# Kernel tuning notes

Measured on AMD Instinct MI355X. Metric: run time of the kernel, lower is better.

Reference implementation:

```python
import jax, jax.numpy as jnp
import numpy as np

B, T, V, E, H, S, C, VF, A, L = 32, 32, 32000, 512, 512, 512, 256, 512, 256, 50


def setup_inputs() -> dict:
    key = jax.random.key(0)
    ks = jax.random.split(key, 17)
    sc = lambda k, shp, fan: (jax.random.normal(k, shp, jnp.float32) / np.sqrt(fan)).astype(jnp.float32)
    inp = {
        "tgt": jax.random.randint(ks[0], (B, T), 0, V, dtype=jnp.int64),
        "decoder_state": jax.random.normal(ks[1], (B, H), jnp.float32),
        "category": jax.random.normal(ks[2], (B, C), jnp.float32),
        "v_feature": jax.random.normal(ks[3], (B, VF), jnp.float32),
        "session_outputs": jax.random.normal(ks[4], (B, L, S), jnp.float32),
        "session_mask": jnp.ones((B, L), dtype=bool),
        # learned parameters
        "emb": sc(ks[5], (V, E), E),
        "attn_Wh": sc(ks[6], (H, A), H),
        "attn_Ws": sc(ks[7], (S, A), S),
        "attn_b": jnp.zeros((A,), jnp.float32),
        "attn_v": sc(ks[8], (A,), A),
        "W_ih": sc(ks[9], (3 * H, E + S + C + VF), H),
        "W_hh": sc(ks[10], (3 * H, H), H),
        "b_ih": jnp.zeros((3 * H,), jnp.float32),
        "b_hh": jnp.zeros((3 * H,), jnp.float32),
        "W_out": 0.1 * jax.random.normal(ks[11], (V, H), jnp.float32),  # init.normal_(0, 0.1)
        "b_out": jnp.zeros((V,), jnp.float32),
    }
    return inp


def reference(tgt, decoder_state, category, v_feature, session_outputs, session_mask,
              emb, attn_Wh, attn_Ws, attn_b, attn_v, W_ih, W_hh, b_ih, b_hh, W_out, b_out):
    neg = jnp.finfo(session_outputs.dtype).min
    x = jnp.swapaxes(emb[tgt], 0, 1)                       # T,B,E
    sess_proj = jnp.einsum('bls,sa->bla', session_outputs, attn_Ws) + attn_b  # precompute key proj

    def step(h, x_t):
        # additive (Bahdanau) session attention on last-layer state h: B,H
        q = (h @ attn_Wh)[:, None, :]                      # B,1,A
        e = jnp.einsum('bla,a->bl', jnp.tanh(q + sess_proj), attn_v)
        e = jnp.where(session_mask, e, neg)
        a = jax.nn.softmax(e, axis=-1)                     # B,L
        ctx = jnp.einsum('bl,blh->bh', a, session_outputs)
        inp = jnp.concatenate([x_t, ctx, category, v_feature], axis=-1)
        # single-step GRU (PyTorch gate order: reset, update, new)
        gx = inp @ W_ih.T + b_ih
        gh = h @ W_hh.T + b_hh
        xr, xz, xn = jnp.split(gx, 3, axis=-1)
        hr, hz, hn = jnp.split(gh, 3, axis=-1)
        r = jax.nn.sigmoid(xr + hr)
        z = jax.nn.sigmoid(xz + hz)
        n = jnp.tanh(xn + r * hn)
        h2 = (1.0 - z) * n + z * h
        vocab = h2 @ W_out.T + b_out
        return h2, (vocab, h2)

    _, (vocab_outputs, outputs) = jax.lax.scan(step, decoder_state, x)
    return jnp.swapaxes(vocab_outputs, 0, 1), jnp.swapaxes(outputs, 0, 1)
```

## Files before the change

### kernel.cpp

```cpp
#include <hip/hip_runtime.h>

typedef unsigned short u16;
typedef unsigned int u32;
typedef __attribute__((ext_vector_type(8))) short short8;
typedef __attribute__((ext_vector_type(4))) float f32x4;

#define NB 32
#define NT 32
#define NV 32000
#define NE 512
#define NH 512
#define NS 512
#define NC 256
#define NVF 512
#define NA 256
#define NL 50
#define G3 1536
#define KG 1024
#define NG 2048

__device__ __forceinline__ float bf2f(u16 u) {
  union { u32 i; float f; } v; v.i = ((u32)u) << 16; return v.f;
}
__device__ __forceinline__ u16 f2bf(float f) {
  union { float f; u32 i; } v; v.f = f;
  u32 x = v.i;
  return (u16)((x + 0x7fffu + ((x >> 16) & 1u)) >> 16);
}
__device__ __forceinline__ float sigmoidf_(float x) { return 1.f / (1.f + __expf(-x)); }
__device__ __forceinline__ float tanhf_(float x) {
  x = fminf(fmaxf(x, -15.f), 15.f);
  float e = __expf(2.f * x);
  return (e - 1.f) / (e + 1.f);
}
__device__ __forceinline__ void cvt8(u16* dst, const float* src) {
  f32x4 a = *(const f32x4*)src;
  f32x4 b = *(const f32x4*)(src + 4);
  short8 o;
  o[0] = (short)f2bf(a[0]); o[1] = (short)f2bf(a[1]);
  o[2] = (short)f2bf(a[2]); o[3] = (short)f2bf(a[3]);
  o[4] = (short)f2bf(b[0]); o[5] = (short)f2bf(b[1]);
  o[6] = (short)f2bf(b[2]); o[7] = (short)f2bf(b[3]);
  *(short8*)dst = o;
}

__global__ __launch_bounds__(256) void prep_kernel(
    const int* __restrict__ tgt, const float* __restrict__ dec,
    const float* __restrict__ cat, const float* __restrict__ vfe,
    const float* __restrict__ sess, const float* __restrict__ emb,
    const float* __restrict__ Ws, const float* __restrict__ Wih,
    const float* __restrict__ Whh, const float* __restrict__ Wout,
    u16* __restrict__ Wg, u16* __restrict__ Wx, u16* __restrict__ X,
    float* __restrict__ h_ws, u16* __restrict__ Wob, u16* __restrict__ Wst,
    u16* __restrict__ sessb, u16* __restrict__ Wcv, u16* __restrict__ cvb)
{
  int blk = blockIdx.x, tid = threadIdx.x;
  if (blk < 1024) {
    int base = (blk * 256 + tid) * 8, j = base >> 10, c = base & 1023;
    if (j < G3 && c < 512)            cvt8(Wg + base, Whh + (size_t)j * 512 + c);
    else if (j < 1024 && c >= 512)    cvt8(Wg + base, Wih + (size_t)j * 1792 + c);
    else if (j >= G3 && c >= 512)     cvt8(Wg + base, Wih + (size_t)(j - 512) * 1792 + c);
    else                              *(short8*)(Wg + base) = (short8){0,0,0,0,0,0,0,0};
  } else if (blk < 1408) {
    int base = ((blk - 1024) * 256 + tid) * 8, j = base >> 9, c = base & 511;
    cvt8(Wx + base, Wih + (size_t)j * 1792 + c);
  } else if (blk < 1664) {
    int base = ((blk - 1408) * 256 + tid) * 8, tb = base >> 9, e = base & 511;
    cvt8(X + base, emb + (size_t)tgt[tb] * NE + e);
  } else if (blk < 1672) {
    int base = ((blk - 1664) * 256 + tid) * 8;
    *(f32x4*)(h_ws + base) = *(const f32x4*)(dec + base);
    *(f32x4*)(h_ws + base + 4) = *(const f32x4*)(dec + base + 4);
  } else if (blk < 9672) {
    int base = ((blk - 1672) * 256 + tid) * 8;
    cvt8(Wob + base, Wout + base);
  } else if (blk < 9736) {
    int base = ((blk - 9672) * 256 + tid) * 8, a = base >> 9, s = base & 511;
    short8 o;
    #pragma unroll
    for (int j = 0; j < 8; j++) o[j] = (short)f2bf(Ws[(size_t)(s + j) * NA + a]);
    *(short8*)(Wst + base) = o;
  } else if (blk < 10136) {
    int base = ((blk - 9736) * 256 + tid) * 8;
    cvt8(sessb + base, sess + base);
  } else if (blk < 10712) {
    int base = ((blk - 10136) * 256 + tid) * 8, j = base / 768, c = base % 768;
    cvt8(Wcv + base, Wih + (size_t)j * 1792 + 1024 + c);
  } else {
    int base = ((blk - 10712) * 256 + tid) * 8, b = base / 768, c = base % 768;
    if (c < NC) cvt8(cvb + base, cat + (size_t)b * NC + c);
    else        cvt8(cvb + base, vfe + (size_t)b * NVF + (c - NC));
  }
}

__global__ __launch_bounds__(256) void att_step(
    int t,
    const float* __restrict__ sess, const float* __restrict__ Wh,
    const float* __restrict__ av, const float* __restrict__ bhh,
    const float* __restrict__ sp, const float* __restrict__ gstat,
    const float* __restrict__ gx, const float* __restrict__ g,
    float* __restrict__ h_ws, u16* __restrict__ A_cur,
    float* __restrict__ h_out, u16* __restrict__ h_bf)
{
  int b = blockIdx.x, tid = threadIdx.x;
  __shared__ float h_s[512];
  __shared__ float qp[2048];
  __shared__ float q_s[256];
  __shared__ float e_s[64];
  __shared__ float a_s[64];

  if (t == 0) {
    h_s[tid] = h_ws[b * NH + tid];
    h_s[256 + tid] = h_ws[b * NH + 256 + tid];
  } else {
    const float* gxr = gx + ((size_t)b * NT + (t - 1)) * G3;
    const float* gr = g + (size_t)b * NG;
    const float* gsr = gstat + (size_t)b * G3;
    #pragma unroll
    for (int s = 0; s < 2; s++) {
      int k = tid + s * 256;
      float hprev = h_ws[b * NH + k];
      float rr = sigmoidf_(gxr[k] + gsr[k] + gr[k] + bhh[k]);
      float zz = sigmoidf_(gxr[512 + k] + gsr[512 + k] + gr[512 + k] + bhh[512 + k]);
      float hn = gr[1024 + k] + bhh[1024 + k];
      float xn = gxr[1024 + k] + gsr[1024 + k] + gr[1536 + k];
      float nn = tanhf_(xn + rr * hn);
      float h2 = (1.f - zz) * nn + zz * hprev;
      h_s[k] = h2;
      h_ws[b * NH + k] = h2;
      h_out[((size_t)b * NT + (t - 1)) * NH + k] = h2;
      h_bf[((size_t)b * NT + (t - 1)) * NH + k] = f2bf(h2);
    }
  }
  __syncthreads();
  if (t == NT) return;

  A_cur[b * KG + tid] = f2bf(h_s[tid]);
  A_cur[b * KG + 256 + tid] = f2bf(h_s[256 + tid]);

  {
    int grp = tid >> 5, lb = tid & 31;
    float qa[8] = {0.f,0.f,0.f,0.f,0.f,0.f,0.f,0.f};
    for (int hh = grp * 64; hh < grp * 64 + 64; hh++) {
      float hv = h_s[hh];
      const float* wr = Wh + (size_t)hh * NA + lb * 8;
      f32x4 w0 = *(const f32x4*)wr;
      f32x4 w1 = *(const f32x4*)(wr + 4);
      qa[0] += hv * w0[0]; qa[1] += hv * w0[1]; qa[2] += hv * w0[2]; qa[3] += hv * w0[3];
      qa[4] += hv * w1[0]; qa[5] += hv * w1[1]; qa[6] += hv * w1[2]; qa[7] += hv * w1[3];
    }
    #pragma unroll
    for (int j = 0; j < 8; j++) qp[grp * 256 + lb * 8 + j] = qa[j];
  }
  __syncthreads();
  {
    float qq = 0.f;
    #pragma unroll
    for (int gg = 0; gg < 8; gg++) qq += qp[gg * 256 + tid];
    q_s[tid] = qq;
  }
  __syncthreads();

  if (tid < 200) {
    int l2 = tid >> 2, grp = tid & 3;
    const float* spr = sp + ((size_t)b * NL + l2) * NA + grp * 64;
    const float* avp = av + grp * 64;
    float part = 0.f;
    for (int j = 0; j < 64; j++)
      part += tanhf_(q_s[grp * 64 + j] + spr[j]) * avp[j];
    part += __shfl_xor(part, 1);
    part += __shfl_xor(part, 2);
    if (grp == 0) e_s[l2] = part;
  }
  __syncthreads();
  if (tid < 64) {
    float x = (tid < NL) ? e_s[tid] : -3.0e38f;
    float m = x;
    #pragma unroll
    for (int o = 1; o < 64; o <<= 1) m = fmaxf(m, __shfl_xor(m, o));
    float p = (tid < NL) ? __expf(x - m) : 0.f;
    float ssum = p;
    #pragma unroll
    for (int o = 1; o < 64; o <<= 1) ssum += __shfl_xor(ssum, o);
    a_s[tid] = p / ssum;
  }
  __syncthreads();

  #pragma unroll
  for (int s0 = 0; s0 < 2; s0++) {
    int s = tid + s0 * 256;
    float acc = 0.f;
    for (int l = 0; l < NL; l++)
      acc += a_s[l] * sess[((size_t)b * NL + l) * NS + s];
    A_cur[b * KG + 512 + s] = f2bf(acc);
  }
}

template<int BM, bool BIAS>
__global__ __launch_bounds__(256) void gemm_bt(
    const u16* __restrict__ Aw, int lda, const u16* __restrict__ Bw, int ldb,
    float* __restrict__ Cw, int ldc, const float* __restrict__ bias, int K, int nblk)
{
  int bn = blockIdx.x % nblk, bm = blockIdx.x / nblk;
  int w = threadIdx.x >> 6, l = threadIdx.x & 63;
  int lr = l & 15, kb = (l >> 4) * 8, r0 = (l >> 4) * 4;
  int n0 = bn * 64 + w * 16;
  constexpr int MT = BM / 16;
  f32x4 acc[MT];
  #pragma unroll
  for (int i = 0; i < MT; i++) acc[i] = (f32x4){0.f, 0.f, 0.f, 0.f};
  const u16* bp = Bw + (size_t)(n0 + lr) * ldb + kb;
  const u16* ap = Aw + (size_t)(bm * BM + lr) * lda + kb;
  #pragma unroll 4
  for (int k0 = 0; k0 < K; k0 += 32) {
    short8 bfr = *(const short8*)(bp + k0);
    #pragma unroll
    for (int mt = 0; mt < MT; mt++) {
      short8 afr = *(const short8*)(ap + (size_t)mt * 16 * lda + k0);
      acc[mt] = __builtin_amdgcn_mfma_f32_16x16x32_bf16(afr, bfr, acc[mt], 0, 0, 0);
    }
  }
  int col = n0 + lr;
  float bv = 0.f;
  if constexpr (BIAS) bv = bias[col];
  #pragma unroll
  for (int mt = 0; mt < MT; mt++) {
    #pragma unroll
    for (int i = 0; i < 4; i++) {
      int row = bm * BM + mt * 16 + r0 + i;
      Cw[(size_t)row * ldc + col] = acc[mt][i] + bv;
    }
  }
}

__global__ __launch_bounds__(256) void vocab_gemm(
    const u16* __restrict__ Aw, const u16* __restrict__ Bw,
    const float* __restrict__ bias, float* __restrict__ Cw)
{
  int bm = blockIdx.x / 250, bn = blockIdx.x % 250;
  int w = threadIdx.x >> 6, l = threadIdx.x & 63;
  int lr = l & 15, kb = (l >> 4) * 8, r0 = (l >> 4) * 4;
  __shared__ __align__(16) u16 As[128 * 136];
  f32x4 acc[8][2];
  #pragma unroll
  for (int i = 0; i < 8; i++) { acc[i][0] = (f32x4){0.f,0.f,0.f,0.f}; acc[i][1] = (f32x4){0.f,0.f,0.f,0.f}; }
  int n0 = bn * 128;
  const u16* bp0 = Bw + (size_t)(n0 + w * 16 + lr) * 512 + kb;
  const u16* bp1 = Bw + (size_t)(n0 + 64 + w * 16 + lr) * 512 + kb;
  for (int ko = 0; ko < 512; ko += 128) {
    __syncthreads();
    #pragma unroll
    for (int it = 0; it < 8; it++) {
      int idx = it * 256 + (int)threadIdx.x;
      int row = idx >> 4, c8 = (idx & 15) * 8;
      *(short8*)(As + row * 136 + c8) = *(const short8*)(Aw + (size_t)(bm * 128 + row) * 512 + ko + c8);
    }
    __syncthreads();
    #pragma unroll
    for (int kc = 0; kc < 128; kc += 32) {
      short8 bf0 = *(const short8*)(bp0 + ko + kc);
      short8 bf1 = *(const short8*)(bp1 + ko + kc);
      #pragma unroll
      for (int mt = 0; mt < 8; mt++) {
        short8 afr = *(const short8*)(As + (mt * 16 + lr) * 136 + kc + kb);
        acc[mt][0] = __builtin_amdgcn_mfma_f32_16x16x32_bf16(afr, bf0, acc[mt][0], 0, 0, 0);
        acc[mt][1] = __builtin_amdgcn_mfma_f32_16x16x32_bf16(afr, bf1, acc[mt][1], 0, 0, 0);
      }
    }
  }
  int col0 = n0 + w * 16 + lr, col1 = col0 + 64;
  float bv0 = bias[col0], bv1 = bias[col1];
  #pragma unroll
  for (int mt = 0; mt < 8; mt++) {
    #pragma unroll
    for (int i = 0; i < 4; i++) {
      int row = bm * 128 + mt * 16 + r0 + i;
      Cw[(size_t)row * NV + col0] = acc[mt][0][i] + bv0;
      Cw[(size_t)row * NV + col1] = acc[mt][1][i] + bv1;
    }
  }
}

extern "C" void kernel_launch(void* const* d_in, const int* in_sizes, int n_in,
                              void* d_out, int out_size, void* d_ws, size_t ws_size,
                              hipStream_t stream)
{
  const int* tgt = (const int*)d_in[0];
  const float* dec = (const float*)d_in[1];
  const float* cat = (const float*)d_in[2];
  const float* vfe = (const float*)d_in[3];
  const float* sess = (const float*)d_in[4];
  const float* emb = (const float*)d_in[6];
  const float* Wh = (const float*)d_in[7];
  const float* Ws = (const float*)d_in[8];
  const float* ab = (const float*)d_in[9];
  const float* av = (const float*)d_in[10];
  const float* Wih = (const float*)d_in[11];
  const float* Whh = (const float*)d_in[12];
  const float* bih = (const float*)d_in[13];
  const float* bhh = (const float*)d_in[14];
  const float* Wout = (const float*)d_in[15];
  const float* bout = (const float*)d_in[16];

  float* out_vocab = (float*)d_out;
  float* h_out = out_vocab + (size_t)NB * NT * NV;

  float* sp = (float*)d_ws;
  float* gstat = sp + NB * NL * NA;
  float* gx = gstat + NB * G3;
  float* g = gx + (size_t)NB * NT * G3;
  float* h_ws = g + NB * NG;
  u16* Wg = (u16*)(h_ws + NB * NH);
  u16* Wx = Wg + (size_t)NG * KG;
  u16* X = Wx + (size_t)G3 * NE;
  u16* A_cur = X + (size_t)NB * NT * NE;
  u16* h_bf = A_cur + NB * KG;
  u16* Wob = h_bf + (size_t)NB * NT * NH;
  u16* Wst = Wob + (size_t)NV * NH;
  u16* sessb = Wst + (size_t)NA * NS;
  u16* Wcv = sessb + (size_t)NB * NL * NS;
  u16* cvb = Wcv + (size_t)G3 * 768;

  prep_kernel<<<10724, 256, 0, stream>>>(tgt, dec, cat, vfe, sess, emb, Ws, Wih, Whh, Wout,
                                         Wg, Wx, X, h_ws, Wob, Wst, sessb, Wcv, cvb);
  gemm_bt<64, false><<<16 * 24, 256, 0, stream>>>(X, 512, Wx, 512, gx, G3, nullptr, 512, 24);
  gemm_bt<64, true><<<25 * 4, 256, 0, stream>>>(sessb, 512, Wst, 512, sp, NA, ab, 512, 4);
  gemm_bt<32, true><<<24, 256, 0, stream>>>(cvb, 768, Wcv, 768, gstat, G3, bih, 768, 24);
  for (int t = 0; t < NT; t++) {
    att_step<<<NB, 256, 0, stream>>>(t, sess, Wh, av, bhh, sp, gstat, gx, g, h_ws, A_cur, h_out, h_bf);
    gemm_bt<32, false><<<32, 256, 0, stream>>>(A_cur, KG, Wg, KG, g, NG, nullptr, KG, 32);
  }
  att_step<<<NB, 256, 0, stream>>>(NT, sess, Wh, av, bhh, sp, gstat, gx, g, h_ws, A_cur, h_out, h_bf);
  vocab_gemm<<<8 * 250, 256, 0, stream>>>(h_bf, Wob, bout, out_vocab);
}
```

Before: 1.348 ms.

## Precompute session-context gate projection and merge query projection into recurrent GEMM

Uses the linearity of the context term to precompute session_outputs @ W_ih[:,512:1024]^T per session position as a bf16 tensor. Each step then mixes these projected rows with the attention weights instead of forming the context and multiplying it by W_ih. The attention query projection W_h is appended to the recurrent GEMM weight, so one GEMM with K=512 yields both the hidden gates and q, shrinking the per-step GEMM from K=1024/N=2048. The vocab GEMM is also retiled to direct-from-global fragments with an LDS-staged coalesced epilogue. The risks are extra bf16 rounding on the precomputed context gates and a large per-step read of the SP2 tensor.

```diff
diff --git a/kernel.cpp b/kernel.cpp
--- a/kernel.cpp
+++ b/kernel.cpp
@@ -16,8 +16,7 @@
 #define NA 256
 #define NL 50
 #define G3 1536
-#define KG 1024
-#define NG 2048
+#define NWB 1792
 
 __device__ __forceinline__ float bf2f(u16 u) {
   union { u32 i; float f; } v; v.i = ((u32)u) << 16; return v.f;
@@ -48,117 +47,79 @@
     const int* __restrict__ tgt, const float* __restrict__ dec,
     const float* __restrict__ cat, const float* __restrict__ vfe,
     const float* __restrict__ sess, const float* __restrict__ emb,
-    const float* __restrict__ Ws, const float* __restrict__ Wih,
-    const float* __restrict__ Whh, const float* __restrict__ Wout,
-    u16* __restrict__ Wg, u16* __restrict__ Wx, u16* __restrict__ X,
-    float* __restrict__ h_ws, u16* __restrict__ Wob, u16* __restrict__ Wst,
-    u16* __restrict__ sessb, u16* __restrict__ Wcv, u16* __restrict__ cvb)
+    const float* __restrict__ Wh, const float* __restrict__ Ws,
+    const float* __restrict__ Wih, const float* __restrict__ Whh,
+    const float* __restrict__ Wout,
+    u16* __restrict__ WB, u16* __restrict__ Wx, u16* __restrict__ Wc,
+    u16* __restrict__ X, u16* __restrict__ Ah, float* __restrict__ h_ws,
+    u16* __restrict__ Wob, u16* __restrict__ Wst, u16* __restrict__ sessb,
+    u16* __restrict__ cvb, u16* __restrict__ Wcv)
 {
   int blk = blockIdx.x, tid = threadIdx.x;
-  if (blk < 1024) {
-    int base = (blk * 256 + tid) * 8, j = base >> 10, c = base & 1023;
-    if (j < G3 && c < 512)            cvt8(Wg + base, Whh + (size_t)j * 512 + c);
-    else if (j < 1024 && c >= 512)    cvt8(Wg + base, Wih + (size_t)j * 1792 + c);
-    else if (j >= G3 && c >= 512)     cvt8(Wg + base, Wih + (size_t)(j - 512) * 1792 + c);
-    else                              *(short8*)(Wg + base) = (short8){0,0,0,0,0,0,0,0};
-  } else if (blk < 1408) {
-    int base = ((blk - 1024) * 256 + tid) * 8, j = base >> 9, c = base & 511;
+  if (blk < 448) {
+    int base = (blk * 256 + tid) * 8, j = base >> 9, c = base & 511;
+    if (j < G3) cvt8(WB + base, Whh + (size_t)j * 512 + c);
+    else {
+      int a = j - G3;
+      short8 o;
+      #pragma unroll
+      for (int i = 0; i < 8; i++) o[i] = (short)f2bf(Wh[(size_t)(c + i) * NA + a]);
+      *(short8*)(WB + base) = o;
+    }
+  } else if (blk < 832) {
+    int base = ((blk - 448) * 256 + tid) * 8, j = base >> 9, c = base & 511;
     cvt8(Wx + base, Wih + (size_t)j * 1792 + c);
-  } else if (blk < 1664) {
-    int base = ((blk - 1408) * 256 + tid) * 8, tb = base >> 9, e = base & 511;
+  } else if (blk < 1216) {
+    int base = ((blk - 832) * 256 + tid) * 8, j = base >> 9, c = base & 511;
+    cvt8(Wc + base, Wih + (size_t)j * 1792 + 512 + c);
+  } else if (blk < 1472) {
+    int base = ((blk - 1216) * 256 + tid) * 8, tb = base >> 9, e = base & 511;
     cvt8(X + base, emb + (size_t)tgt[tb] * NE + e);
-  } else if (blk < 1672) {
-    int base = ((blk - 1664) * 256 + tid) * 8;
+  } else if (blk < 1480) {
+    int base = ((blk - 1472) * 256 + tid) * 8;
+    cvt8(Ah + base, dec + base);
+  } else if (blk < 1488) {
+    int base = ((blk - 1480) * 256 + tid) * 8;
     *(f32x4*)(h_ws + base) = *(const f32x4*)(dec + base);
     *(f32x4*)(h_ws + base + 4) = *(const f32x4*)(dec + base + 4);
-  } else if (blk < 9672) {
-    int base = ((blk - 1672) * 256 + tid) * 8;
+  } else if (blk < 9488) {
+    int base = ((blk - 1488) * 256 + tid) * 8;
     cvt8(Wob + base, Wout + base);
-  } else if (blk < 9736) {
-    int base = ((blk - 9672) * 256 + tid) * 8, a = base >> 9, s = base & 511;
+  } else if (blk < 9552) {
+    int base = ((blk - 9488) * 256 + tid) * 8, a = base >> 9, s = base & 511;
     short8 o;
     #pragma unroll
-    for (int j = 0; j < 8; j++) o[j] = (short)f2bf(Ws[(size_t)(s + j) * NA + a]);
+    for (int i = 0; i < 8; i++) o[i] = (short)f2bf(Ws[(size_t)(s + i) * NA + a]);
     *(short8*)(Wst + base) = o;
-  } else if (blk < 10136) {
-    int base = ((blk - 9736) * 256 + tid) * 8;
+  } else if (blk < 9952) {
+    int base = ((blk - 9552) * 256 + tid) * 8;
     cvt8(sessb + base, sess + base);
-  } else if (blk < 10712) {
-    int base = ((blk - 10136) * 256 + tid) * 8, j = base / 768, c = base % 768;
-    cvt8(Wcv + base, Wih + (size_t)j * 1792 + 1024 + c);
-  } else {
-    int base = ((blk - 10712) * 256 + tid) * 8, b = base / 768, c = base % 768;
+  } else if (blk < 9964) {
+    int base = ((blk - 9952) * 256 + tid) * 8, b = base / 768, c = base % 768;
     if (c < NC) cvt8(cvb + base, cat + (size_t)b * NC + c);
     else        cvt8(cvb + base, vfe + (size_t)b * NVF + (c - NC));
-  }
-}
-
-__global__ __launch_bounds__(256) void att_step(
+  } else {
+    int base = ((blk - 9964) * 256 + tid) * 8, j = base / 768, c = base % 768;
+    cvt8(Wcv + base, Wih + (size_t)j * 1792 + 1024 + c);
+  }
+}
+
+__global__ __launch_bounds__(256) void att_step2(
     int t,
-    const float* __restrict__ sess, const float* __restrict__ Wh,
-    const float* __restrict__ av, const float* __restrict__ bhh,
-    const float* __restrict__ sp, const float* __restrict__ gstat,
-    const float* __restrict__ gx, const float* __restrict__ g,
-    float* __restrict__ h_ws, u16* __restrict__ A_cur,
+    const float* __restrict__ sp, const float* __restrict__ av,
+    const u16* __restrict__ SP2, const float* __restrict__ g2,
+    const float* __restrict__ gx, const float* __restrict__ gstat,
+    const float* __restrict__ bhh,
+    float* __restrict__ h_ws, u16* __restrict__ Ah,
     float* __restrict__ h_out, u16* __restrict__ h_bf)
 {
   int b = blockIdx.x, tid = threadIdx.x;
-  __shared__ float h_s[512];
-  __shared__ float qp[2048];
   __shared__ float q_s[256];
   __shared__ float e_s[64];
   __shared__ float a_s[64];
-
-  if (t == 0) {
-    h_s[tid] = h_ws[b * NH + tid];
-    h_s[256 + tid] = h_ws[b * NH + 256 + tid];
-  } else {
-    const float* gxr = gx + ((size_t)b * NT + (t - 1)) * G3;
-    const float* gr = g + (size_t)b * NG;
-    const float* gsr = gstat + (size_t)b * G3;
-    #pragma unroll
-    for (int s = 0; s < 2; s++) {
-      int k = tid + s * 256;
-      float hprev = h_ws[b * NH + k];
-      float rr = sigmoidf_(gxr[k] + gsr[k] + gr[k] + bhh[k]);
-      float zz = sigmoidf_(gxr[512 + k] + gsr[512 + k] + gr[512 + k] + bhh[512 + k]);
-      float hn = gr[1024 + k] + bhh[1024 + k];
-      float xn = gxr[1024 + k] + gsr[1024 + k] + gr[1536 + k];
-      float nn = tanhf_(xn + rr * hn);
-      float h2 = (1.f - zz) * nn + zz * hprev;
-      h_s[k] = h2;
-      h_ws[b * NH + k] = h2;
-      h_out[((size_t)b * NT + (t - 1)) * NH + k] = h2;
-      h_bf[((size_t)b * NT + (t - 1)) * NH + k] = f2bf(h2);
-    }
-  }
-  __syncthreads();
-  if (t == NT) return;
-
-  A_cur[b * KG + tid] = f2bf(h_s[tid]);
-  A_cur[b * KG + 256 + tid] = f2bf(h_s[256 + tid]);
-
-  {
-    int grp = tid >> 5, lb = tid & 31;
-    float qa[8] = {0.f,0.f,0.f,0.f,0.f,0.f,0.f,0.f};
-    for (int hh = grp * 64; hh < grp * 64 + 64; hh++) {
-      float hv = h_s[hh];
-      const float* wr = Wh + (size_t)hh * NA + lb * 8;
-      f32x4 w0 = *(const f32x4*)wr;
-      f32x4 w1 = *(const f32x4*)(wr + 4);
-      qa[0] += hv * w0[0]; qa[1] += hv * w0[1]; qa[2] += hv * w0[2]; qa[3] += hv * w0[3];
-      qa[4] += hv * w1[0]; qa[5] += hv * w1[1]; qa[6] += hv * w1[2]; qa[7] += hv * w1[3];
-    }
-    #pragma unroll
-    for (int j = 0; j < 8; j++) qp[grp * 256 + lb * 8 + j] = qa[j];
-  }
-  __syncthreads();
-  {
-    float qq = 0.f;
-    #pragma unroll
-    for (int gg = 0; gg < 8; gg++) qq += qp[gg * 256 + tid];
-    q_s[tid] = qq;
-  }
+  __shared__ float gc_s[G3];
+
+  q_s[tid] = g2[(size_t)b * NWB + G3 + tid];
   __syncthreads();
 
   if (tid < 200) {
@@ -166,6 +127,7 @@
     const float* spr = sp + ((size_t)b * NL + l2) * NA + grp * 64;
     const float* avp = av + grp * 64;
     float part = 0.f;
+    #pragma unroll 8
     for (int j = 0; j < 64; j++)
       part += tanhf_(q_s[grp * 64 + j] + spr[j]) * avp[j];
     part += __shfl_xor(part, 1);
@@ -186,20 +148,45 @@
   }
   __syncthreads();
 
-  #pragma unroll
-  for (int s0 = 0; s0 < 2; s0++) {
-    int s = tid + s0 * 256;
-    float acc = 0.f;
-    for (int l = 0; l < NL; l++)
-      acc += a_s[l] * sess[((size_t)b * NL + l) * NS + s];
-    A_cur[b * KG + 512 + s] = f2bf(acc);
-  }
-}
-
-template<int BM, bool BIAS>
+  {
+    const u16* sp2b = SP2 + (size_t)b * NL * G3;
+    #pragma unroll
+    for (int s = 0; s < 6; s++) {
+      int j = s * 256 + tid;
+      float acc = 0.f;
+      #pragma unroll 5
+      for (int l = 0; l < NL; l++)
+        acc += a_s[l] * bf2f(sp2b[(size_t)l * G3 + j]);
+      gc_s[j] = acc;
+    }
+  }
+  __syncthreads();
+
+  const float* gxr = gx + ((size_t)b * NT + t) * G3;
+  const float* gsr = gstat + (size_t)b * G3;
+  const float* ghr = g2 + (size_t)b * NWB;
+  #pragma unroll
+  for (int s = 0; s < 2; s++) {
+    int k = tid + s * 256;
+    float hprev = h_ws[b * NH + k];
+    float rr = sigmoidf_(gxr[k] + gsr[k] + ghr[k] + gc_s[k] + bhh[k]);
+    float zz = sigmoidf_(gxr[512 + k] + gsr[512 + k] + ghr[512 + k] + gc_s[512 + k] + bhh[512 + k]);
+    float hn = ghr[1024 + k] + bhh[1024 + k];
+    float xn = gxr[1024 + k] + gsr[1024 + k] + gc_s[1024 + k];
+    float nn = tanhf_(xn + rr * hn);
+    float h2 = (1.f - zz) * nn + zz * hprev;
+    u16 hb = f2bf(h2);
+    h_ws[b * NH + k] = h2;
+    Ah[b * NH + k] = hb;
+    h_out[((size_t)b * NT + t) * NH + k] = h2;
+    h_bf[((size_t)b * NT + t) * NH + k] = hb;
+  }
+}
+
+template<int BM, bool BIAS, typename OutT>
 __global__ __launch_bounds__(256) void gemm_bt(
     const u16* __restrict__ Aw, int lda, const u16* __restrict__ Bw, int ldb,
-    float* __restrict__ Cw, int ldc, const float* __restrict__ bias, int K, int nblk)
+    OutT* __restrict__ Cw, int ldc, const float* __restrict__ bias, int K, int nblk)
 {
   int bn = blockIdx.x % nblk, bm = blockIdx.x / nblk;
   int w = threadIdx.x >> 6, l = threadIdx.x & 63;
@@ -228,7 +215,9 @@
     #pragma unroll
     for (int i = 0; i < 4; i++) {
       int row = bm * BM + mt * 16 + r0 + i;
-      Cw[(size_t)row * ldc + col] = acc[mt][i] + bv;
+      float v = acc[mt][i] + bv;
+      if constexpr (sizeof(OutT) == 2) Cw[(size_t)row * ldc + col] = f2bf(v);
+      else                             Cw[(size_t)row * ldc + col] = v;
     }
   }
 }
@@ -237,46 +226,52 @@
     const u16* __restrict__ Aw, const u16* __restrict__ Bw,
     const float* __restrict__ bias, float* __restrict__ Cw)
 {
-  int bm = blockIdx.x / 250, bn = blockIdx.x % 250;
-  int w = threadIdx.x >> 6, l = threadIdx.x & 63;
+  int bn = blockIdx.x % 500, bm = blockIdx.x / 500;
+  int tid = threadIdx.x;
+  int w = tid >> 6, l = tid & 63;
   int lr = l & 15, kb = (l >> 4) * 8, r0 = (l >> 4) * 4;
-  __shared__ __align__(16) u16 As[128 * 136];
-  f32x4 acc[8][2];
-  #pragma unroll
-  for (int i = 0; i < 8; i++) { acc[i][0] = (f32x4){0.f,0.f,0.f,0.f}; acc[i][1] = (f32x4){0.f,0.f,0.f,0.f}; }
-  int n0 = bn * 128;
-  const u16* bp0 = Bw + (size_t)(n0 + w * 16 + lr) * 512 + kb;
-  const u16* bp1 = Bw + (size_t)(n0 + 64 + w * 16 + lr) * 512 + kb;
-  for (int ko = 0; ko < 512; ko += 128) {
+  int n0 = bn * 64;
+  int m0 = bm * 256 + w * 64;
+  f32x4 acc[4][4];
+  #pragma unroll
+  for (int i = 0; i < 4; i++)
+    #pragma unroll
+    for (int j = 0; j < 4; j++) acc[i][j] = (f32x4){0.f, 0.f, 0.f, 0.f};
+  const u16* ap = Aw + (size_t)(m0 + lr) * 512 + kb;
+  const u16* bp = Bw + (size_t)(n0 + lr) * 512 + kb;
+  #pragma unroll 2
+  for (int k0 = 0; k0 < 512; k0 += 32) {
+    short8 bfr[4], afr[4];
+    #pragma unroll
+    for (int nt = 0; nt < 4; nt++) bfr[nt] = *(const short8*)(bp + (size_t)nt * 16 * 512 + k0);
+    #pragma unroll
+    for (int mt = 0; mt < 4; mt++) afr[mt] = *(const short8*)(ap + (size_t)mt * 16 * 512 + k0);
+    #pragma unroll
+    for (int mt = 0; mt < 4; mt++)
+      #pragma unroll
+      for (int nt = 0; nt < 4; nt++)
+        acc[mt][nt] = __builtin_amdgcn_mfma_f32_16x16x32_bf16(afr[mt], bfr[nt], acc[mt][nt], 0, 0, 0);
+  }
+  __shared__ float cs[64 * 68];
+  int crow = tid >> 4, ccol = (tid & 15) * 4;
+  f32x4 bb = *(const f32x4*)(bias + n0 + ccol);
+  #pragma unroll
+  for (int g = 0; g < 4; g++) {
     __syncthreads();
     #pragma unroll
-    for (int it = 0; it < 8; it++) {
-      int idx = it * 256 + (int)threadIdx.x;
-      int row = idx >> 4, c8 = (idx & 15) * 8;
-      *(short8*)(As + row * 136 + c8) = *(const short8*)(Aw + (size_t)(bm * 128 + row) * 512 + ko + c8);
-    }
+    for (int nt = 0; nt < 4; nt++)
+      #pragma unroll
+      for (int i = 0; i < 4; i++)
+        cs[(w * 16 + r0 + i) * 68 + nt * 16 + lr] = acc[g][nt][i];
     __syncthreads();
     #pragma unroll
-    for (int kc = 0; kc < 128; kc += 32) {
-      short8 bf0 = *(const short8*)(bp0 + ko + kc);
-      short8 bf1 = *(const short8*)(bp1 + ko + kc);
-      #pragma unroll
-      for (int mt = 0; mt < 8; mt++) {
-        short8 afr = *(const short8*)(As + (mt * 16 + lr) * 136 + kc + kb);
-        acc[mt][0] = __builtin_amdgcn_mfma_f32_16x16x32_bf16(afr, bf0, acc[mt][0], 0, 0, 0);
-        acc[mt][1] = __builtin_amdgcn_mfma_f32_16x16x32_bf16(afr, bf1, acc[mt][1], 0, 0, 0);
-      }
-    }
-  }
-  int col0 = n0 + w * 16 + lr, col1 = col0 + 64;
-  float bv0 = bias[col0], bv1 = bias[col1];
-  #pragma unroll
-  for (int mt = 0; mt < 8; mt++) {
-    #pragma unroll
     for (int i = 0; i < 4; i++) {
-      int row = bm * 128 + mt * 16 + r0 + i;
-      Cw[(size_t)row * NV + col0] = acc[mt][0][i] + bv0;
-      Cw[(size_t)row * NV + col1] = acc[mt][1][i] + bv1;
+      int s = crow * 4 + i;
+      int ww = s >> 4;
+      int grow = bm * 256 + ww * 64 + g * 16 + (s & 15);
+      f32x4 v = *(f32x4*)(cs + s * 68 + ccol);
+      v[0] += bb[0]; v[1] += bb[1]; v[2] += bb[2]; v[3] += bb[3];
+      *(f32x4*)(Cw + (size_t)grow * NV + n0 + ccol) = v;
     }
   }
 }
@@ -308,28 +303,31 @@
   float* sp = (float*)d_ws;
   float* gstat = sp + NB * NL * NA;
   float* gx = gstat + NB * G3;
-  float* g = gx + (size_t)NB * NT * G3;
-  float* h_ws = g + NB * NG;
-  u16* Wg = (u16*)(h_ws + NB * NH);
-  u16* Wx = Wg + (size_t)NG * KG;
-  u16* X = Wx + (size_t)G3 * NE;
-  u16* A_cur = X + (size_t)NB * NT * NE;
-  u16* h_bf = A_cur + NB * KG;
-  u16* Wob = h_bf + (size_t)NB * NT * NH;
+  float* g2 = gx + (size_t)NB * NT * G3;
+  float* h_ws = g2 + NB * NWB;
+  u16* WB = (u16*)(h_ws + NB * NH);
+  u16* Wx = WB + (size_t)NWB * 512;
+  u16* Wc = Wx + (size_t)G3 * 512;
+  u16* X = Wc + (size_t)G3 * 512;
+  u16* Ah = X + (size_t)NB * NT * NE;
+  u16* SP2 = Ah + NB * NH;
+  u16* Wob = SP2 + (size_t)NB * NL * G3;
   u16* Wst = Wob + (size_t)NV * NH;
   u16* sessb = Wst + (size_t)NA * NS;
-  u16* Wcv = sessb + (size_t)NB * NL * NS;
-  u16* cvb = Wcv + (size_t)G3 * 768;
-
-  prep_kernel<<<10724, 256, 0, stream>>>(tgt, dec, cat, vfe, sess, emb, Ws, Wih, Whh, Wout,
-                                         Wg, Wx, X, h_ws, Wob, Wst, sessb, Wcv, cvb);
-  gemm_bt<64, false><<<16 * 24, 256, 0, stream>>>(X, 512, Wx, 512, gx, G3, nullptr, 512, 24);
-  gemm_bt<64, true><<<25 * 4, 256, 0, stream>>>(sessb, 512, Wst, 512, sp, NA, ab, 512, 4);
-  gemm_bt<32, true><<<24, 256, 0, stream>>>(cvb, 768, Wcv, 768, gstat, G3, bih, 768, 24);
+  u16* cvb = sessb + (size_t)NB * NL * NS;
+  u16* Wcv = cvb + NB * 768;
+  u16* h_bf = Wcv + (size_t)G3 * 768;
+
+  prep_kernel<<<10540, 256, 0, stream>>>(tgt, dec, cat, vfe, sess, emb, Wh, Ws, Wih, Whh, Wout,
+                                         WB, Wx, Wc, X, Ah, h_ws, Wob, Wst, sessb, cvb, Wcv);
+  gemm_bt<64, false, float><<<16 * 24, 256, 0, stream>>>(X, 512, Wx, 512, gx, G3, nullptr, 512, 24);
+  gemm_bt<64, true, float><<<25 * 4, 256, 0, stream>>>(sessb, 512, Wst, 512, sp, NA, ab, 512, 4);
+  gemm_bt<32, true, float><<<24, 256, 0, stream>>>(cvb, 768, Wcv, 768, gstat, G3, bih, 768, 24);
+  gemm_bt<64, false, u16><<<25 * 24, 256, 0, stream>>>(sessb, 512, Wc, 512, SP2, G3, nullptr, 512, 24);
+
   for (int t = 0; t < NT; t++) {
-    att_step<<<NB, 256, 0, stream>>>(t, sess, Wh, av, bhh, sp, gstat, gx, g, h_ws, A_cur, h_out, h_bf);
-    gemm_bt<32, false><<<32, 256, 0, stream>>>(A_cur, KG, Wg, KG, g, NG, nullptr, KG, 32);
-  }
-  att_step<<<NB, 256, 0, stream>>>(NT, sess, Wh, av, bhh, sp, gstat, gx, g, h_ws, A_cur, h_out, h_bf);
-  vocab_gemm<<<8 * 250, 256, 0, stream>>>(h_bf, Wob, bout, out_vocab);
-}
+    gemm_bt<32, false, float><<<28, 256, 0, stream>>>(Ah, 512, WB, 512, g2, NWB, nullptr, 512, 28);
+    att_step2<<<NB, 256, 0, stream>>>(t, sp, av, SP2, g2, gx, gstat, bhh, h_ws, Ah, h_out, h_bf);
+  }
+  vocab_gemm<<<4 * 500, 256, 0, stream>>>(h_bf, Wob, bout, out_vocab);
+}
```

Result: faster. 1.265 ms (-6.1%).
